# Kernel optimization log

Hardware: AMD Instinct MI355X
Metric: run time of the kernel (lower is better)

Reference implementation:

```python
import jax, jax.numpy as jnp
import numpy as np

NUM_CLASSES = 2
THRESHOLD = 0.35   # overlap_thresh
NEG_POS = 7        # negative:positive mining ratio
VAR0, VAR1 = 0.1, 0.2  # self.variance


def point_form(boxes):
    # (cx,cy,w,h) -> (xmin,ymin,xmax,ymax); boxes [P,4]
    return jnp.concatenate([boxes[:, :2] - boxes[:, 2:] / 2,
                            boxes[:, :2] + boxes[:, 2:] / 2], axis=1)


def jaccard(box_a, box_b):
    # box_a [B,O,4] xyxy, box_b [P,4] xyxy -> IoU [B,O,P]
    max_xy = jnp.minimum(box_a[:, :, None, 2:], box_b[None, None, :, 2:])
    min_xy = jnp.maximum(box_a[:, :, None, :2], box_b[None, None, :, :2])
    wh = jnp.clip(max_xy - min_xy, 0.0)
    inter = wh[..., 0] * wh[..., 1]
    area_a = ((box_a[..., 2] - box_a[..., 0]) * (box_a[..., 3] - box_a[..., 1]))[:, :, None]
    area_b = ((box_b[:, 2] - box_b[:, 0]) * (box_b[:, 3] - box_b[:, 1]))[None, None, :]
    return inter / (area_a + area_b - inter)


def encode(matched, priors):
    # matched [B,P,4] xyxy, priors [1,P,4] cxcywh -> offsets [B,P,4]
    g_cxcy = (matched[..., :2] + matched[..., 2:]) / 2 - priors[..., :2]
    g_cxcy = g_cxcy / (VAR0 * priors[..., 2:])
    g_wh = (matched[..., 2:] - matched[..., :2]) / priors[..., 2:]
    g_wh = jnp.log(g_wh) / VAR1
    return jnp.concatenate([g_cxcy, g_wh], axis=-1)


def match(truths, labels, priors):
    # truths [B,O,4] xyxy, labels [B,O] float, priors [P,4] cxcywh
    overlaps = jaccard(truths, point_form(priors))      # [B,O,P]
    best_prior_idx = jnp.argmax(overlaps, axis=2)       # [B,O] best prior per gt
    best_truth_overlap = jnp.max(overlaps, axis=1)      # [B,P]
    best_truth_idx = jnp.argmax(overlaps, axis=1)       # [B,P] best gt per prior
    O = truths.shape[1]

    def fix(bto, bti, bpi):
        # ensure every gt keeps its best prior (index_fill_ / loop in torch)
        bto = bto.at[bpi].set(2.0)
        bti = bti.at[bpi].set(jnp.arange(O))
        return bto, bti

    best_truth_overlap, best_truth_idx = jax.vmap(fix)(
        best_truth_overlap, best_truth_idx, best_prior_idx)
    matched = jnp.take_along_axis(truths, best_truth_idx[..., None], axis=1)  # [B,P,4]
    conf = jnp.take_along_axis(labels, best_truth_idx, axis=1).astype(jnp.int32) + 1
    conf = jnp.where(best_truth_overlap < THRESHOLD, 0, conf)  # background
    loc = encode(matched, priors[None])
    return loc, conf


def setup_inputs() -> dict:
    key = jax.random.key(0)
    k1, k2, k3, k4, k5, k6 = jax.random.split(key, 6)
    B, P, O, C = 32, 32768, 32, NUM_CLASSES
    loc_data = jax.random.normal(k1, (B, P, 4), jnp.float32)
    conf_data = jax.random.normal(k2, (B, P, C), jnp.float32)
    # priors: (cx,cy,w,h) in [0,1], wh in [0.02,0.3]
    p_cxcy = jax.random.uniform(k3, (P, 2), jnp.float32)
    p_wh = 0.02 + 0.28 * jax.random.uniform(k4, (P, 2), jnp.float32)
    priors = jnp.concatenate([p_cxcy, p_wh], axis=1)
    # targets: valid xyxy boxes + label column (label 0 -> class 1 after +1)
    t_cxcy = 0.1 + 0.8 * jax.random.uniform(k5, (B, O, 2), jnp.float32)
    t_wh = 0.05 + 0.2 * jax.random.uniform(k6, (B, O, 2), jnp.float32)
    boxes = jnp.concatenate([t_cxcy - t_wh / 2, t_cxcy + t_wh / 2], axis=2)
    labels = jnp.zeros((B, O, 1), jnp.float32)
    targets = jnp.concatenate([boxes, labels], axis=2)
    return {"loc_data": loc_data, "conf_data": conf_data,
            "priors": priors, "targets": targets}


def reference(loc_data, conf_data, priors, targets):
    B, P, C = conf_data.shape
    truths = targets[..., :4]
    labels = targets[..., 4]
    loc_t, conf_t = match(truths, labels, priors)   # [B,P,4], [B,P] int
    pos = conf_t > 0                                # [B,P]

    # localization: smooth-L1 summed over positives
    diff = loc_data - loc_t
    ad = jnp.abs(diff)
    sl1 = jnp.where(ad < 1.0, 0.5 * diff * diff, ad - 0.5)
    loss_l = jnp.sum(sl1 * pos[..., None].astype(loc_data.dtype))

    # per-prior CE loss for hard-negative mining
    lse = jax.nn.logsumexp(conf_data, axis=2)                            # [B,P]
    picked = jnp.take_along_axis(conf_data, conf_t[..., None], axis=2)[..., 0]
    ce = lse - picked                                                    # [B,P]
    mine = jnp.where(pos, 0.0, ce)
    # double-argsort rank trick (descending)
    loss_idx = jnp.argsort(-mine, axis=1)
    idx_rank = jnp.argsort(loss_idx, axis=1)
    num_pos = jnp.sum(pos, axis=1, keepdims=True)                        # [B,1]
    num_neg = jnp.minimum(NEG_POS * num_pos, P - 1)
    neg = idx_rank < num_neg

    sel = pos | neg
    loss_c = jnp.sum(jnp.where(sel, ce, 0.0))

    N = jnp.maximum(jnp.sum(num_pos).astype(jnp.float32), 1.0)
    return loss_l / N, loss_c / N
```

## Files before the change

kernel.cpp:

```cpp
#include <hip/hip_runtime.h>
#include <stdint.h>

#define NB 32
#define NP 32768
#define NO 32
#define THRESH 0.35f
#define NT1 64

typedef unsigned long long u64;
typedef unsigned int u32;

__device__ __forceinline__ float iou_corners(float px1, float py1, float px2, float py2, float ab,
                                             float tx1, float ty1, float tx2, float ty2, float aa)
{
#pragma clang fp contract(off)
    float iw = fminf(tx2, px2) - fmaxf(tx1, px1);
    float ih = fminf(ty2, py2) - fmaxf(ty1, py1);
    iw = fmaxf(iw, 0.f); ih = fmaxf(ih, 0.f);
    float inter = iw * ih;
    return __fdividef(inter, aa + ab - inter);
}

__device__ __forceinline__ float smooth_l1_sum(float4 ld, float4 pr, float4 tt)
{
#pragma clang fp contract(off)
    float g0 = __fdividef((tt.x + tt.z) * 0.5f - pr.x, 0.1f * pr.z);
    float g1 = __fdividef((tt.y + tt.w) * 0.5f - pr.y, 0.1f * pr.w);
    float g2 = __logf(__fdividef(tt.z - tt.x, pr.z)) * 5.0f;
    float g3 = __logf(__fdividef(tt.w - tt.y, pr.w)) * 5.0f;
    float d0 = ld.x - g0, d1 = ld.y - g1, d2 = ld.z - g2, d3 = ld.w - g3;
    float a0 = fabsf(d0), a1 = fabsf(d1), a2 = fabsf(d2), a3 = fabsf(d3);
    return (a0 < 1.f ? 0.5f * d0 * d0 : a0 - 0.5f)
         + (a1 < 1.f ? 0.5f * d1 * d1 : a1 - 0.5f)
         + (a2 < 1.f ? 0.5f * d2 * d2 : a2 - 0.5f)
         + (a3 < 1.f ? 0.5f * d3 * d3 : a3 - 0.5f);
}

__device__ __forceinline__ float lse2(float c0, float c1)
{
#pragma clang fp contract(off)
    float mm = fmaxf(c0, c1), mn = fminf(c0, c1);
    return mm + __logf(1.f + __expf(mn - mm));
}

__global__ __launch_bounds__(256) void kern1(
        const float* __restrict__ loc, const float* __restrict__ conf,
        const float* __restrict__ priors, const float* __restrict__ targets,
        float* __restrict__ mine, u64* __restrict__ bpk_part,
        float* __restrict__ part_sl1, float* __restrict__ part_cep, int* __restrict__ part_np,
        float* __restrict__ sl_tot, float* __restrict__ c_tot,
        int* __restrict__ np_tot, int* __restrict__ done_cnt)
{
#pragma clang fp contract(off)
    __shared__ __align__(16) float4 tbc[NO];
    __shared__ float ta[NO], tlab[NO];
    __shared__ u64 keys[NO];
    __shared__ float rs0[4], rs1[4];
    __shared__ int rc[4];
    const int b = blockIdx.y, x = blockIdx.x, tid = threadIdx.x;
    if (b == 0 && x == 0 && tid == 0) {
        *sl_tot = 0.f; *c_tot = 0.f; *np_tot = 0; *done_cnt = 0;
    }
    if (tid < NO * 5) {
        int o = tid / 5, c = tid % 5;
        float v = targets[b * NO * 5 + tid];
        if (c < 4) ((float*)&tbc[o])[c] = v; else tlab[o] = v;
    }
    if (tid < NO) keys[tid] = 0ull;
    __syncthreads();
    if (tid < NO) {
        float4 t = tbc[tid];
        ta[tid] = (t.z - t.x) * (t.w - t.y);
    }
    __syncthreads();

    const int p0 = x * 512 + tid * 2;
    float4 pr[2];
    float px1[2], py1[2], px2[2], py2[2], ab[2];
#pragma unroll
    for (int j = 0; j < 2; ++j) {
        pr[j] = ((const float4*)priors)[p0 + j];
        px1[j] = pr[j].x - pr[j].z * 0.5f;
        py1[j] = pr[j].y - pr[j].w * 0.5f;
        px2[j] = pr[j].x + pr[j].z * 0.5f;
        py2[j] = pr[j].y + pr[j].w * 0.5f;
        ab[j]  = pr[j].z * pr[j].w;
    }
    u64 bk[2] = {0ull, 0ull};
    const int lane_o = tid & 31;
    for (int it = 0; it < NO; ++it) {
        const int o = (it + lane_o) & 31;
        float4 tt = tbc[o];
        float aa = ta[o];
        float iou2[2];
#pragma unroll
        for (int j = 0; j < 2; ++j) {
            float iou = iou_corners(px1[j], py1[j], px2[j], py2[j], ab[j],
                                    tt.x, tt.y, tt.z, tt.w, aa);
            iou2[j] = iou;
            u64 ko = ((u64)__float_as_uint(iou) << 6) | (u64)(63 - o);
            bk[j] = bk[j] > ko ? bk[j] : ko;
        }
        float vm = fmaxf(iou2[0], iou2[1]);
        u64 cur = keys[o];
        if (__float_as_uint(vm) > (u32)(cur >> 32)) {
            float bi = iou2[1]; int bp = p0 + 1;
            if (iou2[0] >= bi) { bi = iou2[0]; bp = p0; }
            atomicMax(&keys[o], ((u64)__float_as_uint(bi) << 32) | (u64)(~(u32)bp));
        }
    }

    const size_t gbase = (size_t)b * NP + p0;
    float4 cf = ((const float4*)conf)[gbase >> 1];
    float c0[2] = {cf.x, cf.z};
    float c1[2] = {cf.y, cf.w};
    float2 mout;
    float s_sl1 = 0.f, s_cep = 0.f;
    int np = 0;
#pragma unroll
    for (int j = 0; j < 2; ++j) {
        u32 vb = (u32)(bk[j] >> 6);
        float bv = __uint_as_float(vb);
        int o = 63 - (int)(bk[j] & 63);
        int cfv = (bv < THRESH) ? 0 : ((int)tlab[o] + 1);
        bool pos = cfv > 0;
        float4 ld = ((const float4*)loc)[gbase + j];
        float sl1 = smooth_l1_sum(ld, pr[j], tbc[o]);
        float ce = lse2(c0[j], c1[j]) - ((cfv == 0) ? c0[j] : c1[j]);
        if (pos) { s_sl1 += sl1; s_cep += ce; np++; }
        ((float*)&mout)[j] = pos ? 0.f : ce;
    }
    ((float2*)mine)[gbase >> 1] = mout;

#pragma unroll
    for (int m = 32; m; m >>= 1) {
        s_sl1 += __shfl_xor(s_sl1, m, 64);
        s_cep += __shfl_xor(s_cep, m, 64);
        np    += __shfl_xor(np, m, 64);
    }
    int lane = tid & 63, w = tid >> 6;
    if (lane == 0) { rs0[w] = s_sl1; rs1[w] = s_cep; rc[w] = np; }
    __syncthreads();
    if (tid == 0) {
        float t0 = 0.f, t1 = 0.f; int t2 = 0;
        for (int i = 0; i < 4; ++i) { t0 += rs0[i]; t1 += rs1[i]; t2 += rc[i]; }
        part_sl1[b * NT1 + x] = t0;
        part_cep[b * NT1 + x] = t1;
        part_np [b * NT1 + x] = t2;
    }
    if (tid < NO) bpk_part[(b * NT1 + x) * 32 + tid] = keys[tid];
}

#define HCOL 33
__global__ __launch_bounds__(1024) void kern3(
        const float* __restrict__ loc, const float* __restrict__ conf,
        const float* __restrict__ priors, const float* __restrict__ targets,
        const u64* __restrict__ bpk_part, const float* __restrict__ mine,
        const float* __restrict__ part_sl1, const float* __restrict__ part_cep,
        const int* __restrict__ part_np,
        float* __restrict__ sl_tot, float* __restrict__ c_tot,
        int* __restrict__ np_tot, int* __restrict__ done_cnt,
        float* __restrict__ out)
{
#pragma clang fp contract(off)
    const int b = blockIdx.x, tid = threadIdx.x;
    const int wave = tid >> 6, lane = tid & 63;
    const int cl = lane & 31;
    __shared__ __align__(16) float4 tbc[NO];
    __shared__ float tlab[NO], tas[NO];
    __shared__ u32 pp[NO];
    __shared__ u32 flags[1024];
    __shared__ int hist[256 * HCOL];
    __shared__ int total[256];
    __shared__ float rs[16];
    __shared__ int rc2[16];
    __shared__ float sh_sl1, sh_cep;
    __shared__ int sh_np, sh_k, sh_kk;
    __shared__ u32 sh_prefix;

    if (tid < NO * 5) {
        int o = tid / 5, c = tid % 5;
        float v = targets[b * NO * 5 + tid];
        if (c < 4) ((float*)&tbc[o])[c] = v; else tlab[o] = v;
    }
    flags[tid] = 0u;
    for (int i = tid; i < 256 * HCOL; i += 1024) hist[i] = 0;

    const float* mb = mine + (size_t)b * NP;
    float v[32];
#pragma unroll
    for (int q = 0; q < 8; ++q) {
        float4 t4 = ((const float4*)mb)[q * 1024 + tid];
        v[4 * q] = t4.x; v[4 * q + 1] = t4.y; v[4 * q + 2] = t4.z; v[4 * q + 3] = t4.w;
    }
    __syncthreads();
#pragma unroll 8
    for (int j = 0; j < 32; ++j)
        atomicAdd(&hist[(__float_as_uint(v[j]) >> 24) * HCOL + cl], 1);
    if (tid < NO) {
        float4 t = tbc[tid];
        tas[tid] = (t.z - t.x) * (t.w - t.y);
        u64 key = 0ull;
        for (int xx = 0; xx < NT1; ++xx) {
            u64 t2 = bpk_part[(b * NT1 + xx) * 32 + tid];
            key = t2 > key ? t2 : key;
        }
        pp[tid] = (key >> 32) ? ~(u32)key : 0u;
    }
    __syncthreads();
    if (tid < NO) {
        const int o = tid;
        const u32 p = pp[o];
        float dsl1 = 0.f, dcep = 0.f; int dnp = 0;
        bool last = true;
        for (int o2 = o + 1; o2 < NO; ++o2)
            if (pp[o2] == p) { last = false; break; }
        if (last) {
            float4 prr = ((const float4*)priors)[p];
            float px1 = prr.x - prr.z * 0.5f, py1 = prr.y - prr.w * 0.5f;
            float px2 = prr.x + prr.z * 0.5f, py2 = prr.y + prr.w * 0.5f;
            float ab = prr.z * prr.w;
            float bv = -1.f; int bo_ = 0;
            for (int o2 = 0; o2 < NO; ++o2) {
                float4 t2 = tbc[o2];
                float i2 = iou_corners(px1, py1, px2, py2, ab, t2.x, t2.y, t2.z, t2.w, tas[o2]);
                if (i2 > bv) { bv = i2; bo_ = o2; }
            }
            int cf_pre = (bv < THRESH) ? 0 : ((int)tlab[bo_] + 1);
            size_t gp = (size_t)b * NP + p;
            float4 ld = ((const float4*)loc)[gp];
            float2 c = ((const float2*)conf)[gp];
            float lse = lse2(c.x, c.y);
            int cf_new = (int)tlab[o] + 1;
            dsl1 = smooth_l1_sum(ld, prr, tbc[o]);
            dcep = lse - ((cf_new == 0) ? c.x : c.y);
            dnp = 1;
            if (cf_pre > 0) {
                dsl1 -= smooth_l1_sum(ld, prr, tbc[bo_]);
                dcep -= lse - ((cf_pre == 0) ? c.x : c.y);
                dnp = 0;
            }
            float oldv = mb[p];
            atomicSub(&hist[(__float_as_uint(oldv) >> 24) * HCOL + cl], 1);
            atomicAdd(&hist[cl], 1);
            atomicOr(&flags[p >> 5], 1u << (p & 31));
        }
        float a = part_sl1[b * NT1 + o] + part_sl1[b * NT1 + 32 + o] + dsl1;
        float d = part_cep[b * NT1 + o] + part_cep[b * NT1 + 32 + o] + dcep;
        int   n = part_np [b * NT1 + o] + part_np [b * NT1 + 32 + o] + dnp;
#pragma unroll
        for (int m = 16; m; m >>= 1) {
            a += __shfl_xor(a, m, 32);
            d += __shfl_xor(d, m, 32);
            n += __shfl_xor(n, m, 32);
        }
        if (o == 0) {
            sh_sl1 = a; sh_cep = d; sh_np = n;
            sh_k = min(7 * n, NP - 1); sh_kk = sh_k; sh_prefix = 0u;
        }
    }
    __syncthreads();
#pragma unroll
    for (int q = 0; q < 8; ++q) {
        u32 word = flags[q * 128 + (tid >> 3)];
#pragma unroll
        for (int c = 0; c < 4; ++c)
            if ((word >> (((tid & 7) << 2) + c)) & 1u) v[4 * q + c] = 0.f;
    }
    const int k = sh_k;
    float topk = 0.f;
    if (k > 0) {
        for (int pass = 0; pass < 4; ++pass) {
            if (pass > 0) {
                for (int i = tid; i < 256 * HCOL; i += 1024) hist[i] = 0;
                __syncthreads();
                const int shift = 24 - 8 * pass;
                const u32 pfx = sh_prefix;
#pragma unroll 8
                for (int j = 0; j < 32; ++j) {
                    u32 kb = __float_as_uint(v[j]);
                    if ((u32)(((u64)kb) >> (shift + 8)) == pfx)
                        atomicAdd(&hist[((kb >> shift) & 255) * HCOL + cl], 1);
                }
                __syncthreads();
            }
            if (tid < 512) {
                int bin = tid >> 1;
                const int base = bin * HCOL + (tid & 1) * 16;
                int s = 0;
#pragma unroll
                for (int i = 0; i < 16; ++i) s += hist[base + i];
                s += __shfl_xor(s, 1, 64);
                if ((tid & 1) == 0) total[bin] = s;
            }
            __syncthreads();
            if (tid < 64) {
                int4 h4 = ((const int4*)total)[tid];
                int s3 = h4.w, s2 = h4.z + s3, s1 = h4.y + s2, s0 = h4.x + s1;
                int acc = s0;
#pragma unroll
                for (int off = 1; off < 64; off <<= 1) {
                    int u = __shfl_down(acc, off, 64);
                    if (tid + off < 64) acc += u;
                }
                int excl = acc - s0;
                int kk = sh_kk;
                int cand = -1, nkk = 0;
                if (excl + s3 >= kk)      { cand = 4 * tid + 3; nkk = kk - excl; }
                else if (excl + s2 >= kk) { cand = 4 * tid + 2; nkk = kk - excl - s3; }
                else if (excl + s1 >= kk) { cand = 4 * tid + 1; nkk = kk - excl - s2; }
                else if (excl + s0 >= kk) { cand = 4 * tid + 0; nkk = kk - excl - s1; }
                int cmax = cand;
#pragma unroll
                for (int off = 1; off < 64; off <<= 1) cmax = max(cmax, __shfl_xor(cmax, off, 64));
                if (cand >= 0 && cand == cmax) {
                    sh_prefix = (sh_prefix << 8) | (u32)(cand & 255);
                    sh_kk = nkk;
                }
            }
            __syncthreads();
        }
        const u32 T = sh_prefix;
        const float tval = __uint_as_float(T);
        float s = 0.f; int c2 = 0;
#pragma unroll
        for (int j = 0; j < 32; ++j) {
            if (__float_as_uint(v[j]) > T) { s += v[j]; c2++; }
        }
#pragma unroll
        for (int m = 32; m; m >>= 1) {
            s  += __shfl_xor(s, m, 64);
            c2 += __shfl_xor(c2, m, 64);
        }
        if (lane == 0) { rs[wave] = s; rc2[wave] = c2; }
        __syncthreads();
        if (tid == 0) {
            float st = 0.f; int ct = 0;
            for (int i = 0; i < 16; ++i) { st += rs[i]; ct += rc2[i]; }
            topk = st + (float)(k - ct) * tval;
        }
    }
    if (tid == 0) {
        atomicAdd(sl_tot, sh_sl1);
        atomicAdd(c_tot, sh_cep + topk);
        atomicAdd(np_tot, sh_np);
        __threadfence();
        int d = atomicAdd(done_cnt, 1);
        if (d == NB - 1) {
            float sl = atomicAdd(sl_tot, 0.f);
            float cc = atomicAdd(c_tot, 0.f);
            int   np = atomicAdd(np_tot, 0);
            float N = fmaxf((float)np, 1.f);
            out[0] = sl / N;
            out[1] = cc / N;
        }
    }
}

extern "C" void kernel_launch(void* const* d_in, const int* in_sizes, int n_in,
                              void* d_out, int out_size, void* d_ws, size_t ws_size,
                              hipStream_t stream) {
    const float* loc     = (const float*)d_in[0];
    const float* conf    = (const float*)d_in[1];
    const float* priors  = (const float*)d_in[2];
    const float* targets = (const float*)d_in[3];
    float* out = (float*)d_out;

    char* ws = (char*)d_ws;
    float* mine     = (float*)ws;
    u64*   bpk_part = (u64*)(ws + 4194304);
    float* part_sl1 = (float*)(ws + 4718592);
    float* part_cep = (float*)(ws + 4726784);
    int*   part_np  = (int*)(ws + 4734976);
    float* sl_tot   = (float*)(ws + 4743168);
    float* c_tot    = (float*)(ws + 4743172);
    int*   np_tot   = (int*)(ws + 4743176);
    int*   done_cnt = (int*)(ws + 4743180);

    dim3 g1(NT1, NB);
    kern1<<<g1, 256, 0, stream>>>(loc, conf, priors, targets, mine, bpk_part,
                                  part_sl1, part_cep, part_np,
                                  sl_tot, c_tot, np_tot, done_cnt);
    kern3<<<NB, 1024, 0, stream>>>(loc, conf, priors, targets, bpk_part, mine,
                                   part_sl1, part_cep, part_np,
                                   sl_tot, c_tot, np_tot, done_cnt, out);
}
```

Baseline: 127.2 us.

## Fuse match and top-k kernels via last-block-per-batch completion counter

Merges the two kernels into one launch. Per-batch partial sums and best-prior keys are combined with global atomics, and the last block to finish each batch runs the radix-select top-k over the mine buffer, which it re-reads from global memory with 256 threads instead of holding it in registers across 1024 threads. A memset is added to zero the counters. The aim is to remove a kernel launch and the partial-buffer reduction. The cost is that the tail work runs serially per batch in a smaller block, with four global passes over the mine buffer, which may lengthen the critical path.

```diff
diff --git a/kernel.cpp b/kernel.cpp
--- a/kernel.cpp
+++ b/kernel.cpp
@@ -43,13 +43,16 @@
     return mm + __logf(1.f + __expf(mn - mm));
 }
 
-__global__ __launch_bounds__(256) void kern1(
+#define HCOL 17
+__global__ __launch_bounds__(256, 8) void kern_fused(
         const float* __restrict__ loc, const float* __restrict__ conf,
         const float* __restrict__ priors, const float* __restrict__ targets,
-        float* __restrict__ mine, u64* __restrict__ bpk_part,
-        float* __restrict__ part_sl1, float* __restrict__ part_cep, int* __restrict__ part_np,
+        float* __restrict__ mine, u64* __restrict__ bpk,
+        int* __restrict__ batch_done,
+        float* __restrict__ batch_sl1, float* __restrict__ batch_cep, int* __restrict__ batch_np,
         float* __restrict__ sl_tot, float* __restrict__ c_tot,
-        int* __restrict__ np_tot, int* __restrict__ done_cnt)
+        int* __restrict__ np_tot, int* __restrict__ done_cnt,
+        float* __restrict__ out)
 {
 #pragma clang fp contract(off)
     __shared__ __align__(16) float4 tbc[NO];
@@ -57,10 +60,17 @@
     __shared__ u64 keys[NO];
     __shared__ float rs0[4], rs1[4];
     __shared__ int rc[4];
+    __shared__ int hist[256 * HCOL];
+    __shared__ int total[256];
+    __shared__ u32 pp[NO];
+    __shared__ float rs[4];
+    __shared__ int rc2[4];
+    __shared__ float sh_sl1, sh_cep;
+    __shared__ int sh_np, sh_k, sh_kk, sh_sel;
+    __shared__ u32 sh_prefix;
+
     const int b = blockIdx.y, x = blockIdx.x, tid = threadIdx.x;
-    if (b == 0 && x == 0 && tid == 0) {
-        *sl_tot = 0.f; *c_tot = 0.f; *np_tot = 0; *done_cnt = 0;
-    }
+    const int lane = tid & 63, wave = tid >> 6;
     if (tid < NO * 5) {
         int o = tid / 5, c = tid % 5;
         float v = targets[b * NO * 5 + tid];
@@ -138,73 +148,26 @@
         s_cep += __shfl_xor(s_cep, m, 64);
         np    += __shfl_xor(np, m, 64);
     }
-    int lane = tid & 63, w = tid >> 6;
-    if (lane == 0) { rs0[w] = s_sl1; rs1[w] = s_cep; rc[w] = np; }
+    if (lane == 0) { rs0[wave] = s_sl1; rs1[wave] = s_cep; rc[wave] = np; }
+    if (tid < NO) atomicMax(&bpk[b * NO + tid], keys[tid]);
     __syncthreads();
     if (tid == 0) {
         float t0 = 0.f, t1 = 0.f; int t2 = 0;
         for (int i = 0; i < 4; ++i) { t0 += rs0[i]; t1 += rs1[i]; t2 += rc[i]; }
-        part_sl1[b * NT1 + x] = t0;
-        part_cep[b * NT1 + x] = t1;
-        part_np [b * NT1 + x] = t2;
-    }
-    if (tid < NO) bpk_part[(b * NT1 + x) * 32 + tid] = keys[tid];
-}
-
-#define HCOL 33
-__global__ __launch_bounds__(1024) void kern3(
-        const float* __restrict__ loc, const float* __restrict__ conf,
-        const float* __restrict__ priors, const float* __restrict__ targets,
-        const u64* __restrict__ bpk_part, const float* __restrict__ mine,
-        const float* __restrict__ part_sl1, const float* __restrict__ part_cep,
-        const int* __restrict__ part_np,
-        float* __restrict__ sl_tot, float* __restrict__ c_tot,
-        int* __restrict__ np_tot, int* __restrict__ done_cnt,
-        float* __restrict__ out)
-{
-#pragma clang fp contract(off)
-    const int b = blockIdx.x, tid = threadIdx.x;
-    const int wave = tid >> 6, lane = tid & 63;
-    const int cl = lane & 31;
-    __shared__ __align__(16) float4 tbc[NO];
-    __shared__ float tlab[NO], tas[NO];
-    __shared__ u32 pp[NO];
-    __shared__ u32 flags[1024];
-    __shared__ int hist[256 * HCOL];
-    __shared__ int total[256];
-    __shared__ float rs[16];
-    __shared__ int rc2[16];
-    __shared__ float sh_sl1, sh_cep;
-    __shared__ int sh_np, sh_k, sh_kk;
-    __shared__ u32 sh_prefix;
-
-    if (tid < NO * 5) {
-        int o = tid / 5, c = tid % 5;
-        float v = targets[b * NO * 5 + tid];
-        if (c < 4) ((float*)&tbc[o])[c] = v; else tlab[o] = v;
-    }
-    flags[tid] = 0u;
-    for (int i = tid; i < 256 * HCOL; i += 1024) hist[i] = 0;
-
-    const float* mb = mine + (size_t)b * NP;
-    float v[32];
-#pragma unroll
-    for (int q = 0; q < 8; ++q) {
-        float4 t4 = ((const float4*)mb)[q * 1024 + tid];
-        v[4 * q] = t4.x; v[4 * q + 1] = t4.y; v[4 * q + 2] = t4.z; v[4 * q + 3] = t4.w;
-    }
-    __syncthreads();
-#pragma unroll 8
-    for (int j = 0; j < 32; ++j)
-        atomicAdd(&hist[(__float_as_uint(v[j]) >> 24) * HCOL + cl], 1);
+        atomicAdd(&batch_sl1[b], t0);
+        atomicAdd(&batch_cep[b], t1);
+        atomicAdd(&batch_np[b], t2);
+        __threadfence();
+        int done = atomicAdd(&batch_done[b], 1);
+        sh_sel = (done == NT1 - 1) ? 1 : 0;
+    }
+    __syncthreads();
+    if (!sh_sel) return;
+
+    __threadfence();
+    __syncthreads();
     if (tid < NO) {
-        float4 t = tbc[tid];
-        tas[tid] = (t.z - t.x) * (t.w - t.y);
-        u64 key = 0ull;
-        for (int xx = 0; xx < NT1; ++xx) {
-            u64 t2 = bpk_part[(b * NT1 + xx) * 32 + tid];
-            key = t2 > key ? t2 : key;
-        }
+        u64 key = bpk[b * NO + tid];
         pp[tid] = (key >> 32) ? ~(u32)key : 0u;
     }
     __syncthreads();
@@ -217,13 +180,14 @@
             if (pp[o2] == p) { last = false; break; }
         if (last) {
             float4 prr = ((const float4*)priors)[p];
-            float px1 = prr.x - prr.z * 0.5f, py1 = prr.y - prr.w * 0.5f;
-            float px2 = prr.x + prr.z * 0.5f, py2 = prr.y + prr.w * 0.5f;
-            float ab = prr.z * prr.w;
+            float qx1 = prr.x - prr.z * 0.5f, qy1 = prr.y - prr.w * 0.5f;
+            float qx2 = prr.x + prr.z * 0.5f, qy2 = prr.y + prr.w * 0.5f;
+            float qab = prr.z * prr.w;
             float bv = -1.f; int bo_ = 0;
             for (int o2 = 0; o2 < NO; ++o2) {
                 float4 t2 = tbc[o2];
-                float i2 = iou_corners(px1, py1, px2, py2, ab, t2.x, t2.y, t2.z, t2.w, tas[o2]);
+                float aa2 = (t2.z - t2.x) * (t2.w - t2.y);
+                float i2 = iou_corners(qx1, qy1, qx2, qy2, qab, t2.x, t2.y, t2.z, t2.w, aa2);
                 if (i2 > bv) { bv = i2; bo_ = o2; }
             }
             int cf_pre = (bv < THRESH) ? 0 : ((int)tlab[bo_] + 1);
@@ -240,58 +204,50 @@
                 dcep -= lse - ((cf_pre == 0) ? c.x : c.y);
                 dnp = 0;
             }
-            float oldv = mb[p];
-            atomicSub(&hist[(__float_as_uint(oldv) >> 24) * HCOL + cl], 1);
-            atomicAdd(&hist[cl], 1);
-            atomicOr(&flags[p >> 5], 1u << (p & 31));
-        }
-        float a = part_sl1[b * NT1 + o] + part_sl1[b * NT1 + 32 + o] + dsl1;
-        float d = part_cep[b * NT1 + o] + part_cep[b * NT1 + 32 + o] + dcep;
-        int   n = part_np [b * NT1 + o] + part_np [b * NT1 + 32 + o] + dnp;
+            mine[gp] = 0.f;
+        }
 #pragma unroll
         for (int m = 16; m; m >>= 1) {
-            a += __shfl_xor(a, m, 32);
-            d += __shfl_xor(d, m, 32);
-            n += __shfl_xor(n, m, 32);
+            dsl1 += __shfl_xor(dsl1, m, 32);
+            dcep += __shfl_xor(dcep, m, 32);
+            dnp  += __shfl_xor(dnp, m, 32);
         }
         if (o == 0) {
+            float a = atomicAdd(&batch_sl1[b], 0.f) + dsl1;
+            float d = atomicAdd(&batch_cep[b], 0.f) + dcep;
+            int   n = atomicAdd(&batch_np[b], 0)   + dnp;
             sh_sl1 = a; sh_cep = d; sh_np = n;
             sh_k = min(7 * n, NP - 1); sh_kk = sh_k; sh_prefix = 0u;
         }
     }
     __syncthreads();
-#pragma unroll
-    for (int q = 0; q < 8; ++q) {
-        u32 word = flags[q * 128 + (tid >> 3)];
-#pragma unroll
-        for (int c = 0; c < 4; ++c)
-            if ((word >> (((tid & 7) << 2) + c)) & 1u) v[4 * q + c] = 0.f;
-    }
     const int k = sh_k;
     float topk = 0.f;
+    const float* mb = mine + (size_t)b * NP;
+    const int cl = lane & (HCOL - 2);
     if (k > 0) {
         for (int pass = 0; pass < 4; ++pass) {
-            if (pass > 0) {
-                for (int i = tid; i < 256 * HCOL; i += 1024) hist[i] = 0;
-                __syncthreads();
-                const int shift = 24 - 8 * pass;
-                const u32 pfx = sh_prefix;
-#pragma unroll 8
-                for (int j = 0; j < 32; ++j) {
-                    u32 kb = __float_as_uint(v[j]);
+#pragma unroll
+            for (int i = 0; i < HCOL; ++i) hist[i * 256 + tid] = 0;
+            __syncthreads();
+            const int shift = 24 - 8 * pass;
+            const u32 pfx = sh_prefix;
+            for (int j = 0; j < 32; ++j) {
+                float4 t4 = ((const float4*)mb)[j * 256 + tid];
+#pragma unroll
+                for (int c = 0; c < 4; ++c) {
+                    u32 kb = __float_as_uint(((const float*)&t4)[c]);
                     if ((u32)(((u64)kb) >> (shift + 8)) == pfx)
                         atomicAdd(&hist[((kb >> shift) & 255) * HCOL + cl], 1);
                 }
-                __syncthreads();
-            }
-            if (tid < 512) {
-                int bin = tid >> 1;
-                const int base = bin * HCOL + (tid & 1) * 16;
+            }
+            __syncthreads();
+            {
                 int s = 0;
-#pragma unroll
-                for (int i = 0; i < 16; ++i) s += hist[base + i];
-                s += __shfl_xor(s, 1, 64);
-                if ((tid & 1) == 0) total[bin] = s;
+                const int base = tid * HCOL;
+#pragma unroll
+                for (int i = 0; i < HCOL - 1; ++i) s += hist[base + i];
+                total[tid] = s;
             }
             __syncthreads();
             if (tid < 64) {
@@ -314,7 +270,7 @@
 #pragma unroll
                 for (int off = 1; off < 64; off <<= 1) cmax = max(cmax, __shfl_xor(cmax, off, 64));
                 if (cand >= 0 && cand == cmax) {
-                    sh_prefix = (sh_prefix << 8) | (u32)(cand & 255);
+                    sh_prefix = (pfx << 8) | (u32)(cand & 255);
                     sh_kk = nkk;
                 }
             }
@@ -323,9 +279,13 @@
         const u32 T = sh_prefix;
         const float tval = __uint_as_float(T);
         float s = 0.f; int c2 = 0;
-#pragma unroll
         for (int j = 0; j < 32; ++j) {
-            if (__float_as_uint(v[j]) > T) { s += v[j]; c2++; }
+            float4 t4 = ((const float4*)mb)[j * 256 + tid];
+#pragma unroll
+            for (int c = 0; c < 4; ++c) {
+                float vv = ((const float*)&t4)[c];
+                if (__float_as_uint(vv) > T) { s += vv; c2++; }
+            }
         }
 #pragma unroll
         for (int m = 32; m; m >>= 1) {
@@ -336,7 +296,7 @@
         __syncthreads();
         if (tid == 0) {
             float st = 0.f; int ct = 0;
-            for (int i = 0; i < 16; ++i) { st += rs[i]; ct += rc2[i]; }
+            for (int i = 0; i < 4; ++i) { st += rs[i]; ct += rc2[i]; }
             topk = st + (float)(k - ct) * tval;
         }
     }
@@ -349,8 +309,8 @@
         if (d == NB - 1) {
             float sl = atomicAdd(sl_tot, 0.f);
             float cc = atomicAdd(c_tot, 0.f);
-            int   np = atomicAdd(np_tot, 0);
-            float N = fmaxf((float)np, 1.f);
+            int   nn = atomicAdd(np_tot, 0);
+            float N = fmaxf((float)nn, 1.f);
             out[0] = sl / N;
             out[1] = cc / N;
         }
@@ -367,21 +327,20 @@
     float* out = (float*)d_out;
 
     char* ws = (char*)d_ws;
-    float* mine     = (float*)ws;
-    u64*   bpk_part = (u64*)(ws + 4194304);
-    float* part_sl1 = (float*)(ws + 4718592);
-    float* part_cep = (float*)(ws + 4726784);
-    int*   part_np  = (int*)(ws + 4734976);
-    float* sl_tot   = (float*)(ws + 4743168);
-    float* c_tot    = (float*)(ws + 4743172);
-    int*   np_tot   = (int*)(ws + 4743176);
-    int*   done_cnt = (int*)(ws + 4743180);
-
-    dim3 g1(NT1, NB);
-    kern1<<<g1, 256, 0, stream>>>(loc, conf, priors, targets, mine, bpk_part,
-                                  part_sl1, part_cep, part_np,
-                                  sl_tot, c_tot, np_tot, done_cnt);
-    kern3<<<NB, 1024, 0, stream>>>(loc, conf, priors, targets, bpk_part, mine,
-                                   part_sl1, part_cep, part_np,
-                                   sl_tot, c_tot, np_tot, done_cnt, out);
-}
+    u64*   bpk        = (u64*)ws;
+    int*   batch_done = (int*)(ws + 8192);
+    float* batch_sl1  = (float*)(ws + 8320);
+    float* batch_cep  = (float*)(ws + 8448);
+    int*   batch_np   = (int*)(ws + 8576);
+    float* sl_tot     = (float*)(ws + 8704);
+    float* c_tot      = (float*)(ws + 8708);
+    int*   np_tot     = (int*)(ws + 8712);
+    int*   done_cnt   = (int*)(ws + 8716);
+    float* mine       = (float*)(ws + 16384);
+
+    hipMemsetAsync(ws, 0, 8720, stream);
+    dim3 g(NT1, NB);
+    kern_fused<<<g, 256, 0, stream>>>(loc, conf, priors, targets, mine, bpk,
+                                      batch_done, batch_sl1, batch_cep, batch_np,
+                                      sl_tot, c_tot, np_tot, done_cnt, out);
+}
```

Result: slower. 227.1 us (+78.6%).

## Build top-byte histogram and reductions in kern1 via global atomics

Applied to the files above, without the earlier changes.

The first radix-select pass histogram moves from the per-batch kern3 block into kern1, where each block builds a shared histogram and adds it to a global per-batch histogram. Best-prior keys and the per-batch sums now reach global memory through atomics instead of per-block partial arrays that kern3 had to scan. A memset is added to zero the workspace before the launch. The aim is to take the serial 32-value atomic histogram pass and the 64-partial key scan off the 32-block kern3, which underuses the GPU. In exchange kern1 pays for extra shared and global atomics and the launch pays for an extra memset.

```diff
diff --git a/kernel.cpp b/kernel.cpp
--- a/kernel.cpp
+++ b/kernel.cpp
@@ -6,6 +6,7 @@
 #define NO 32
 #define THRESH 0.35f
 #define NT1 64
+#define H1COL 17
 
 typedef unsigned long long u64;
 typedef unsigned int u32;
@@ -46,27 +47,25 @@
 __global__ __launch_bounds__(256) void kern1(
         const float* __restrict__ loc, const float* __restrict__ conf,
         const float* __restrict__ priors, const float* __restrict__ targets,
-        float* __restrict__ mine, u64* __restrict__ bpk_part,
-        float* __restrict__ part_sl1, float* __restrict__ part_cep, int* __restrict__ part_np,
-        float* __restrict__ sl_tot, float* __restrict__ c_tot,
-        int* __restrict__ np_tot, int* __restrict__ done_cnt)
+        float* __restrict__ mine, u64* __restrict__ bpk, int* __restrict__ hist256g,
+        float* __restrict__ batch_sl1, float* __restrict__ batch_cep, int* __restrict__ batch_np)
 {
 #pragma clang fp contract(off)
     __shared__ __align__(16) float4 tbc[NO];
     __shared__ float ta[NO], tlab[NO];
     __shared__ u64 keys[NO];
+    __shared__ int h1[256 * H1COL];
     __shared__ float rs0[4], rs1[4];
     __shared__ int rc[4];
     const int b = blockIdx.y, x = blockIdx.x, tid = threadIdx.x;
-    if (b == 0 && x == 0 && tid == 0) {
-        *sl_tot = 0.f; *c_tot = 0.f; *np_tot = 0; *done_cnt = 0;
-    }
     if (tid < NO * 5) {
         int o = tid / 5, c = tid % 5;
         float v = targets[b * NO * 5 + tid];
         if (c < 4) ((float*)&tbc[o])[c] = v; else tlab[o] = v;
     }
     if (tid < NO) keys[tid] = 0ull;
+#pragma unroll
+    for (int i = 0; i < H1COL; ++i) h1[i * 256 + tid] = 0;
     __syncthreads();
     if (tid < NO) {
         float4 t = tbc[tid];
@@ -131,6 +130,9 @@
         ((float*)&mout)[j] = pos ? 0.f : ce;
     }
     ((float2*)mine)[gbase >> 1] = mout;
+    const int col = tid & 15;
+    atomicAdd(&h1[(__float_as_uint(mout.x) >> 24) * H1COL + col], 1);
+    atomicAdd(&h1[(__float_as_uint(mout.y) >> 24) * H1COL + col], 1);
 
 #pragma unroll
     for (int m = 32; m; m >>= 1) {
@@ -141,23 +143,31 @@
     int lane = tid & 63, w = tid >> 6;
     if (lane == 0) { rs0[w] = s_sl1; rs1[w] = s_cep; rc[w] = np; }
     __syncthreads();
+    if (tid < NO) atomicMax(&bpk[b * NO + tid], keys[tid]);
+    {
+        int s = 0;
+        const int base = tid * H1COL;
+#pragma unroll
+        for (int i = 0; i < 16; ++i) s += h1[base + i];
+        if (s) atomicAdd(&hist256g[b * 256 + tid], s);
+    }
     if (tid == 0) {
         float t0 = 0.f, t1 = 0.f; int t2 = 0;
         for (int i = 0; i < 4; ++i) { t0 += rs0[i]; t1 += rs1[i]; t2 += rc[i]; }
-        part_sl1[b * NT1 + x] = t0;
-        part_cep[b * NT1 + x] = t1;
-        part_np [b * NT1 + x] = t2;
-    }
-    if (tid < NO) bpk_part[(b * NT1 + x) * 32 + tid] = keys[tid];
+        atomicAdd(&batch_sl1[b], t0);
+        atomicAdd(&batch_cep[b], t1);
+        atomicAdd(&batch_np[b], t2);
+    }
 }
 
 #define HCOL 33
 __global__ __launch_bounds__(1024) void kern3(
         const float* __restrict__ loc, const float* __restrict__ conf,
         const float* __restrict__ priors, const float* __restrict__ targets,
-        const u64* __restrict__ bpk_part, const float* __restrict__ mine,
-        const float* __restrict__ part_sl1, const float* __restrict__ part_cep,
-        const int* __restrict__ part_np,
+        const u64* __restrict__ bpk, const float* __restrict__ mine,
+        const int* __restrict__ hist256g,
+        const float* __restrict__ batch_sl1, const float* __restrict__ batch_cep,
+        const int* __restrict__ batch_np,
         float* __restrict__ sl_tot, float* __restrict__ c_tot,
         int* __restrict__ np_tot, int* __restrict__ done_cnt,
         float* __restrict__ out)
@@ -184,8 +194,7 @@
         if (c < 4) ((float*)&tbc[o])[c] = v; else tlab[o] = v;
     }
     flags[tid] = 0u;
-    for (int i = tid; i < 256 * HCOL; i += 1024) hist[i] = 0;
-
+    if (tid < 256) total[tid] = hist256g[b * 256 + tid];
     const float* mb = mine + (size_t)b * NP;
     float v[32];
 #pragma unroll
@@ -193,18 +202,14 @@
         float4 t4 = ((const float4*)mb)[q * 1024 + tid];
         v[4 * q] = t4.x; v[4 * q + 1] = t4.y; v[4 * q + 2] = t4.z; v[4 * q + 3] = t4.w;
     }
-    __syncthreads();
-#pragma unroll 8
-    for (int j = 0; j < 32; ++j)
-        atomicAdd(&hist[(__float_as_uint(v[j]) >> 24) * HCOL + cl], 1);
+    if (tid < NO) {
+        float4 t = tbc[tid];
+    }
+    __syncthreads();
     if (tid < NO) {
         float4 t = tbc[tid];
         tas[tid] = (t.z - t.x) * (t.w - t.y);
-        u64 key = 0ull;
-        for (int xx = 0; xx < NT1; ++xx) {
-            u64 t2 = bpk_part[(b * NT1 + xx) * 32 + tid];
-            key = t2 > key ? t2 : key;
-        }
+        u64 key = bpk[b * NO + tid];
         pp[tid] = (key >> 32) ? ~(u32)key : 0u;
     }
     __syncthreads();
@@ -217,13 +222,13 @@
             if (pp[o2] == p) { last = false; break; }
         if (last) {
             float4 prr = ((const float4*)priors)[p];
-            float px1 = prr.x - prr.z * 0.5f, py1 = prr.y - prr.w * 0.5f;
-            float px2 = prr.x + prr.z * 0.5f, py2 = prr.y + prr.w * 0.5f;
-            float ab = prr.z * prr.w;
+            float qx1 = prr.x - prr.z * 0.5f, qy1 = prr.y - prr.w * 0.5f;
+            float qx2 = prr.x + prr.z * 0.5f, qy2 = prr.y + prr.w * 0.5f;
+            float qab = prr.z * prr.w;
             float bv = -1.f; int bo_ = 0;
             for (int o2 = 0; o2 < NO; ++o2) {
                 float4 t2 = tbc[o2];
-                float i2 = iou_corners(px1, py1, px2, py2, ab, t2.x, t2.y, t2.z, t2.w, tas[o2]);
+                float i2 = iou_corners(qx1, qy1, qx2, qy2, qab, t2.x, t2.y, t2.z, t2.w, tas[o2]);
                 if (i2 > bv) { bv = i2; bo_ = o2; }
             }
             int cf_pre = (bv < THRESH) ? 0 : ((int)tlab[bo_] + 1);
@@ -241,20 +246,20 @@
                 dnp = 0;
             }
             float oldv = mb[p];
-            atomicSub(&hist[(__float_as_uint(oldv) >> 24) * HCOL + cl], 1);
-            atomicAdd(&hist[cl], 1);
+            atomicSub(&total[__float_as_uint(oldv) >> 24], 1);
+            atomicAdd(&total[0], 1);
             atomicOr(&flags[p >> 5], 1u << (p & 31));
         }
-        float a = part_sl1[b * NT1 + o] + part_sl1[b * NT1 + 32 + o] + dsl1;
-        float d = part_cep[b * NT1 + o] + part_cep[b * NT1 + 32 + o] + dcep;
-        int   n = part_np [b * NT1 + o] + part_np [b * NT1 + 32 + o] + dnp;
 #pragma unroll
         for (int m = 16; m; m >>= 1) {
-            a += __shfl_xor(a, m, 32);
-            d += __shfl_xor(d, m, 32);
-            n += __shfl_xor(n, m, 32);
+            dsl1 += __shfl_xor(dsl1, m, 32);
+            dcep += __shfl_xor(dcep, m, 32);
+            dnp  += __shfl_xor(dnp, m, 32);
         }
         if (o == 0) {
+            float a = batch_sl1[b] + dsl1;
+            float d = batch_cep[b] + dcep;
+            int   n = batch_np[b]  + dnp;
             sh_sl1 = a; sh_cep = d; sh_np = n;
             sh_k = min(7 * n, NP - 1); sh_kk = sh_k; sh_prefix = 0u;
         }
@@ -283,17 +288,17 @@
                         atomicAdd(&hist[((kb >> shift) & 255) * HCOL + cl], 1);
                 }
                 __syncthreads();
+                if (tid < 512) {
+                    int bin = tid >> 1;
+                    const int base = bin * HCOL + (tid & 1) * 16;
+                    int s = 0;
+#pragma unroll
+                    for (int i = 0; i < 16; ++i) s += hist[base + i];
+                    s += __shfl_xor(s, 1, 64);
+                    if ((tid & 1) == 0) total[bin] = s;
+                }
+                __syncthreads();
             }
-            if (tid < 512) {
-                int bin = tid >> 1;
-                const int base = bin * HCOL + (tid & 1) * 16;
-                int s = 0;
-#pragma unroll
-                for (int i = 0; i < 16; ++i) s += hist[base + i];
-                s += __shfl_xor(s, 1, 64);
-                if ((tid & 1) == 0) total[bin] = s;
-            }
-            __syncthreads();
             if (tid < 64) {
                 int4 h4 = ((const int4*)total)[tid];
                 int s3 = h4.w, s2 = h4.z + s3, s1 = h4.y + s2, s0 = h4.x + s1;
@@ -349,8 +354,8 @@
         if (d == NB - 1) {
             float sl = atomicAdd(sl_tot, 0.f);
             float cc = atomicAdd(c_tot, 0.f);
-            int   np = atomicAdd(np_tot, 0);
-            float N = fmaxf((float)np, 1.f);
+            int   nn = atomicAdd(np_tot, 0);
+            float N = fmaxf((float)nn, 1.f);
             out[0] = sl / N;
             out[1] = cc / N;
         }
@@ -367,21 +372,22 @@
     float* out = (float*)d_out;
 
     char* ws = (char*)d_ws;
-    float* mine     = (float*)ws;
-    u64*   bpk_part = (u64*)(ws + 4194304);
-    float* part_sl1 = (float*)(ws + 4718592);
-    float* part_cep = (float*)(ws + 4726784);
-    int*   part_np  = (int*)(ws + 4734976);
-    float* sl_tot   = (float*)(ws + 4743168);
-    float* c_tot    = (float*)(ws + 4743172);
-    int*   np_tot   = (int*)(ws + 4743176);
-    int*   done_cnt = (int*)(ws + 4743180);
-
+    u64*   bpk       = (u64*)ws;
+    int*   hist256g  = (int*)(ws + 8192);
+    float* batch_sl1 = (float*)(ws + 40960);
+    float* batch_cep = (float*)(ws + 41088);
+    int*   batch_np  = (int*)(ws + 41216);
+    float* sl_tot    = (float*)(ws + 41344);
+    float* c_tot     = (float*)(ws + 41348);
+    int*   np_tot    = (int*)(ws + 41352);
+    int*   done_cnt  = (int*)(ws + 41356);
+    float* mine      = (float*)(ws + 65536);
+
+    hipMemsetAsync(ws, 0, 41360, stream);
     dim3 g1(NT1, NB);
-    kern1<<<g1, 256, 0, stream>>>(loc, conf, priors, targets, mine, bpk_part,
-                                  part_sl1, part_cep, part_np,
-                                  sl_tot, c_tot, np_tot, done_cnt);
-    kern3<<<NB, 1024, 0, stream>>>(loc, conf, priors, targets, bpk_part, mine,
-                                   part_sl1, part_cep, part_np,
+    kern1<<<g1, 256, 0, stream>>>(loc, conf, priors, targets, mine, bpk, hist256g,
+                                  batch_sl1, batch_cep, batch_np);
+    kern3<<<NB, 1024, 0, stream>>>(loc, conf, priors, targets, bpk, mine, hist256g,
+                                   batch_sl1, batch_cep, batch_np,
                                    sl_tot, c_tot, np_tot, done_cnt, out);
 }
```

Measured after the change: 130.8 us. 1.03x slower.
